# Optimization experiments

Measured on AMD Instinct MI355X. Metric: run time of the kernel, lower is better.

## Reference

```python
import jax, jax.numpy as jnp
import numpy as np

DIM_IN, DIM_Q, DIM_K = 1024, 128, 128
B, S = 8, 2048

def setup_inputs() -> dict:
    key = jax.random.key(0)
    ks = jax.random.split(key, 9)
    sq = 1.0 / np.sqrt(DIM_IN)
    return {
        "query": jax.random.normal(ks[0], (B, S, DIM_IN), jnp.float32),
        "key": jax.random.normal(ks[1], (B, S, DIM_IN), jnp.float32),
        "value": jax.random.normal(ks[2], (B, S, DIM_IN), jnp.float32),
        "Wq": jax.random.uniform(ks[3], (DIM_IN, DIM_Q), jnp.float32, -sq, sq),
        "bq": jax.random.uniform(ks[4], (DIM_Q,), jnp.float32, -sq, sq),
        "Wk": jax.random.uniform(ks[5], (DIM_IN, DIM_K), jnp.float32, -sq, sq),
        "bk": jax.random.uniform(ks[6], (DIM_K,), jnp.float32, -sq, sq),
        "Wv": jax.random.uniform(ks[7], (DIM_IN, DIM_K), jnp.float32, -sq, sq),
        "bv": jax.random.uniform(ks[8], (DIM_K,), jnp.float32, -sq, sq),
    }

def reference(query, key, value, Wq, bq, Wk, bk, Wv, bv):
    q = jnp.einsum("bsd,dq->bsq", query, Wq) + bq          # [B,S,Dq]
    k = jnp.einsum("bsd,dk->bsk", key, Wk) + bk            # [B,S,Dk]
    v = jnp.einsum("bsd,dk->bsk", value, Wv) + bv          # [B,S,Dk]
    scale = jnp.asarray(q.shape[-1] ** 0.5, q.dtype)
    scores = jnp.einsum("bqd,bkd->bqk", q, k) / scale      # [B,S,S]
    attn = jax.nn.softmax(scores, axis=-1)
    return jnp.einsum("bqk,bkd->bqd", attn, v)             # [B,S,Dk]
```

## Files before the change

kernel.cpp:

```cpp
#include <hip/hip_runtime.h>

typedef __attribute__((ext_vector_type(8))) short short8;
typedef __attribute__((ext_vector_type(4))) float floatx4;

#define MFMA16(a, b, c) __builtin_amdgcn_mfma_f32_16x16x32_bf16(a, b, c, 0, 0, 0)

__device__ __forceinline__ short f2bf(float f) {
    unsigned int u = __float_as_uint(f);
    u = u + 0x7fffu + ((u >> 16) & 1u);
    return (short)(u >> 16);
}

__device__ __forceinline__ void ldst16(const void* g, void* l) {
    __builtin_amdgcn_global_load_lds(
        (const __attribute__((address_space(1))) void*)g,
        (__attribute__((address_space(3))) void*)l, 16, 0, 0);
}

__global__ __launch_bounds__(256) void wconv_kernel(const float* __restrict__ Wq,
                                                    const float* __restrict__ Wk,
                                                    const float* __restrict__ Wv,
                                                    short* __restrict__ wtf) {
    int idx = blockIdx.x * 256 + threadIdx.x;
    int w = idx >> 17;
    int rem = idx & 131071;
    int ks = rem >> 12;
    int r2 = rem & 4095;
    int nt = r2 >> 9;
    int r3 = r2 & 511;
    int lane = r3 >> 3, e = r3 & 7;
    int q4 = lane >> 4, l16 = lane & 15;
    int n = 16 * nt + l16;
    int k = 32 * ks + 8 * q4 + e;
    const float* W = (w == 0) ? Wq : (w == 1) ? Wk : Wv;
    wtf[idx] = f2bf(W[k * 128 + n]);
}

__global__ __launch_bounds__(256, 3) void proj_kernel(const float* __restrict__ Q,
                                                      const float* __restrict__ K,
                                                      const float* __restrict__ V,
                                                      const short* __restrict__ wtf,
                                                      const float* __restrict__ bq,
                                                      const float* __restrict__ bk,
                                                      const float* __restrict__ bv,
                                                      short* __restrict__ qo,
                                                      short* __restrict__ ko,
                                                      short* __restrict__ vo) {
    alignas(16) __shared__ float Asl[2][64 * 64];
    const int t = threadIdx.x;
    const int wv = t >> 6, L = t & 63;
    const int wm = wv >> 1, wn = wv & 1;
    const int q4 = L >> 4, l16 = L & 15;
    const int which = blockIdx.y;
    const float* A = (which == 0) ? Q : (which == 1) ? K : V;
    const short* Wf = wtf + which * 131072;
    const float* bias = (which == 0) ? bq : (which == 1) ? bk : bv;
    const int m0 = blockIdx.x * 64;

    floatx4 acc[2][4];
#pragma unroll
    for (int rg = 0; rg < 2; rg++)
#pragma unroll
        for (int nt = 0; nt < 4; nt++) acc[rg][nt] = (floatx4)0.0f;

    auto stage = [&](int buf, int k0) {
#pragma unroll
        for (int j = 0; j < 4; j++) {
            int s = j * 256 + t;
            int r = s >> 4, c = (s & 15) ^ (r & 15);
            ldst16(A + (size_t)(m0 + r) * 1024 + k0 + (c << 2),
                   &Asl[buf][(j * 256 + 64 * wv) * 4]);
        }
    };

    stage(0, 0);

    for (int kc = 0; kc < 16; kc++) {
        const int cur = kc & 1;
        __syncthreads();

        short8 bfr[2][4];
#pragma unroll
        for (int ks = 0; ks < 2; ks++)
#pragma unroll
            for (int nt = 0; nt < 4; nt++)
                bfr[ks][nt] = *(const short8*)(Wf +
                    (((size_t)(2 * kc + ks) * 8 + 4 * wn + nt) * 64 + L) * 8);

        if (kc + 1 < 16) stage(cur ^ 1, (kc + 1) * 64);

        short8 af[2][2];
#pragma unroll
        for (int rg = 0; rg < 2; rg++)
#pragma unroll
            for (int ks = 0; ks < 2; ks++) {
                int r = 32 * wm + 16 * rg + l16;
                int c0 = 8 * ks + 2 * q4;
                float4 f0 = *(float4*)&Asl[cur][(r * 16 + (c0 ^ l16)) * 4];
                float4 f1 = *(float4*)&Asl[cur][(r * 16 + ((c0 + 1) ^ l16)) * 4];
                short8 v;
                v[0] = f2bf(f0.x); v[1] = f2bf(f0.y); v[2] = f2bf(f0.z); v[3] = f2bf(f0.w);
                v[4] = f2bf(f1.x); v[5] = f2bf(f1.y); v[6] = f2bf(f1.z); v[7] = f2bf(f1.w);
                af[rg][ks] = v;
            }
#pragma unroll
        for (int ks = 0; ks < 2; ks++)
#pragma unroll
            for (int nt = 0; nt < 4; nt++) {
                acc[0][nt] = MFMA16(af[0][ks], bfr[ks][nt], acc[0][nt]);
                acc[1][nt] = MFMA16(af[1][ks], bfr[ks][nt], acc[1][nt]);
            }
    }

#pragma unroll
    for (int rg = 0; rg < 2; rg++) {
        const int rbase = m0 + 32 * wm + 16 * rg + q4 * 4;
#pragma unroll
        for (int nt = 0; nt < 4; nt++) {
            const int col = 64 * wn + 16 * nt + l16;
            float bvv = bias[col];
#pragma unroll
            for (int r = 0; r < 4; r++) {
                short h = f2bf(acc[rg][nt][r] + bvv);
                int grow = rbase + r;
                if (which == 0) {
                    qo[(size_t)grow * 128 + col] = h;
                } else if (which == 1) {
                    ko[(size_t)grow * 128 + col] = h;
                } else {
                    int bb = grow >> 11, s = grow & 2047;
                    vo[(size_t)bb * 262144 + (size_t)col * 2048 + s] = h;
                }
            }
        }
    }
}

__global__ __launch_bounds__(512, 2) void flash_kernel(const short* __restrict__ qw,
                                                       const short* __restrict__ kw,
                                                       const short* __restrict__ vw,
                                                       float* __restrict__ out) {
    alignas(16) __shared__ short Kls[2][2][64 * 128];
    alignas(16) __shared__ short Vls[2][2][128 * 64];
    alignas(16) __shared__ short Pl[2][64][72];
    const int t = threadIdx.x;
    const int wvi = t >> 6, L = t & 63;
    const int pr = wvi >> 2, wq = wvi & 3;
    const int pt = t & 255;
    const int q4 = L >> 4, l16 = L & 15;
    const int bid = blockIdx.x;
    const int b = bid & 7, bq = bid >> 3;
    const short* qp = qw + (size_t)b * 262144 + (size_t)bq * 64 * 128;
    const short* kp = kw + (size_t)b * 262144;
    const short* vp = vw + (size_t)b * 262144;

    short8 qf[4];
#pragma unroll
    for (int ks = 0; ks < 4; ks++)
        qf[ks] = *(const short8*)(qp + (16 * wq + l16) * 128 + ks * 32 + q4 * 8);

    floatx4 oacc[8];
#pragma unroll
    for (int dt = 0; dt < 8; dt++) oacc[dt] = (floatx4)0.0f;
    float ps[4] = {0.f, 0.f, 0.f, 0.f};
    const float SL = (float)(0.08838834764831845 * 1.4426950408889634);

    auto stage = [&](int buf, int kt) {
        const int kv0 = pr * 1024 + kt * 64;
#pragma unroll
        for (int j = 0; j < 4; j++) {
            int s = j * 256 + pt;
            int r = s >> 4, c = (s & 15) ^ (r & 15);
            ldst16(kp + (size_t)(kv0 + r) * 128 + c * 8,
                   &Kls[buf][pr][(j * 256 + 64 * wq) * 8]);
        }
#pragma unroll
        for (int j = 0; j < 4; j++) {
            int s = j * 256 + pt;
            int r = s >> 3, c = (s & 7) ^ (r & 7);
            ldst16(vp + (size_t)r * 2048 + kv0 + c * 8,
                   &Vls[buf][pr][(j * 256 + 64 * wq) * 8]);
        }
    };

    stage(0, 0);

    for (int kt = 0; kt < 16; kt++) {
        const int cur = kt & 1;
        __syncthreads();
        if (kt + 1 < 16) stage(cur ^ 1, kt + 1);

        floatx4 sa[4];
#pragma unroll
        for (int nt = 0; nt < 4; nt++) {
            sa[nt] = (floatx4)0.0f;
#pragma unroll
            for (int ks = 0; ks < 4; ks++) {
                short8 bfr = *(short8*)&Kls[cur][pr][(16 * nt + l16) * 128 + ((4 * ks + q4) ^ l16) * 8];
                sa[nt] = MFMA16(qf[ks], bfr, sa[nt]);
            }
        }

#pragma unroll
        for (int nt = 0; nt < 4; nt++) {
#pragma unroll
            for (int r = 0; r < 4; r++) {
                float pv = __builtin_amdgcn_exp2f(sa[nt][r] * SL - 4.0f);
                ps[r] += pv;
                Pl[pr][16 * wq + q4 * 4 + r][16 * nt + l16] = f2bf(pv);
            }
        }

        short8 pf0 = *(short8*)&Pl[pr][16 * wq + l16][q4 * 8];
        short8 pf1 = *(short8*)&Pl[pr][16 * wq + l16][32 + q4 * 8];
#pragma unroll
        for (int dt = 0; dt < 8; dt++) {
            short8 v0 = *(short8*)&Vls[cur][pr][(16 * dt + l16) * 64 + (q4 ^ (l16 & 7)) * 8];
            short8 v1 = *(short8*)&Vls[cur][pr][(16 * dt + l16) * 64 + ((4 + q4) ^ (l16 & 7)) * 8];
            oacc[dt] = MFMA16(pf0, v0, oacc[dt]);
            oacc[dt] = MFMA16(pf1, v1, oacc[dt]);
        }
    }

#pragma unroll
    for (int r = 0; r < 4; r++)
#pragma unroll
        for (int off = 1; off <= 8; off <<= 1)
            ps[r] += __shfl_xor(ps[r], off, 64);

    __syncthreads();
    float* Om = (float*)&Kls[0][0][0];
    float* Lm = (float*)&Vls[0][0][0];
    if (pr == 1) {
#pragma unroll
        for (int dt = 0; dt < 8; dt++)
#pragma unroll
            for (int r = 0; r < 4; r++)
                Om[(16 * wq + q4 * 4 + r) * 128 + 16 * dt + l16] = oacc[dt][r];
        if (l16 == 0)
#pragma unroll
            for (int r = 0; r < 4; r++)
                Lm[16 * wq + q4 * 4 + r] = ps[r];
    }
    __syncthreads();
    if (pr == 0) {
        float inv[4];
#pragma unroll
        for (int r = 0; r < 4; r++)
            inv[r] = 1.0f / (ps[r] + Lm[16 * wq + q4 * 4 + r]);
#pragma unroll
        for (int dt = 0; dt < 8; dt++) {
#pragma unroll
            for (int r = 0; r < 4; r++) {
                int row = 16 * wq + q4 * 4 + r;
                int qrow = bq * 64 + row;
                out[((size_t)b * 2048 + qrow) * 128 + 16 * dt + l16] =
                    (oacc[dt][r] + Om[row * 128 + 16 * dt + l16]) * inv[r];
            }
        }
    }
}

extern "C" void kernel_launch(void* const* d_in, const int* in_sizes, int n_in,
                              void* d_out, int out_size, void* d_ws, size_t ws_size,
                              hipStream_t stream) {
    const float* query = (const float*)d_in[0];
    const float* key   = (const float*)d_in[1];
    const float* value = (const float*)d_in[2];
    const float* Wq    = (const float*)d_in[3];
    const float* bq    = (const float*)d_in[4];
    const float* Wk    = (const float*)d_in[5];
    const float* bk    = (const float*)d_in[6];
    const float* Wv    = (const float*)d_in[7];
    const float* bv    = (const float*)d_in[8];
    float* out = (float*)d_out;

    short* wtf = (short*)d_ws;
    short* qws = wtf + 3 * 131072;
    short* kws = qws + 16384 * 128;
    short* vws = kws + 16384 * 128;

    wconv_kernel<<<1536, 256, 0, stream>>>(Wq, Wk, Wv, wtf);
    proj_kernel<<<dim3(256, 3), 256, 0, stream>>>(query, key, value, wtf,
                                                  bq, bk, bv, qws, kws, vws);
    flash_kernel<<<256, 512, 0, stream>>>(qws, kws, vws, out);
}
```

Baseline: 261.3 us.

## Software-pipeline projection and attention loops with explicit vmcnt waits and setprio

Restructures both the projection GEMM and the attention loop so that the next tile's async LDS loads (and, in the projection, the next weight fragments in a double-buffered register set) are issued before a partial s_waitcnt vmcnt. Raw barriers and sched_barriers replace __syncthreads, and MFMA sections are wrapped in s_setprio to favour matrix issue across waves. The aim is to overlap global-memory latency with compute instead of stalling on a full wait each iteration. This adds hand-counted vmcnt values that must match the number of outstanding loads exactly. It also adds a second barrier per iteration and more register pressure from the two weight buffers.

```diff
diff --git a/kernel.cpp b/kernel.cpp
--- a/kernel.cpp
+++ b/kernel.cpp
@@ -73,22 +73,16 @@
         }
     };
 
-    stage(0, 0);
-
-    for (int kc = 0; kc < 16; kc++) {
-        const int cur = kc & 1;
-        __syncthreads();
-
-        short8 bfr[2][4];
+    auto loadB = [&](int kc, short8 (&dst)[2][4]) {
 #pragma unroll
         for (int ks = 0; ks < 2; ks++)
 #pragma unroll
             for (int nt = 0; nt < 4; nt++)
-                bfr[ks][nt] = *(const short8*)(Wf +
+                dst[ks][nt] = *(const short8*)(Wf +
                     (((size_t)(2 * kc + ks) * 8 + 4 * wn + nt) * 64 + L) * 8);
-
-        if (kc + 1 < 16) stage(cur ^ 1, (kc + 1) * 64);
-
+    };
+
+    auto computeC = [&](int kc, short8 (&bfr)[2][4]) {
         short8 af[2][2];
 #pragma unroll
         for (int rg = 0; rg < 2; rg++)
@@ -96,13 +90,14 @@
             for (int ks = 0; ks < 2; ks++) {
                 int r = 32 * wm + 16 * rg + l16;
                 int c0 = 8 * ks + 2 * q4;
-                float4 f0 = *(float4*)&Asl[cur][(r * 16 + (c0 ^ l16)) * 4];
-                float4 f1 = *(float4*)&Asl[cur][(r * 16 + ((c0 + 1) ^ l16)) * 4];
+                float4 f0 = *(float4*)&Asl[kc & 1][(r * 16 + (c0 ^ l16)) * 4];
+                float4 f1 = *(float4*)&Asl[kc & 1][(r * 16 + ((c0 + 1) ^ l16)) * 4];
                 short8 v;
                 v[0] = f2bf(f0.x); v[1] = f2bf(f0.y); v[2] = f2bf(f0.z); v[3] = f2bf(f0.w);
                 v[4] = f2bf(f1.x); v[5] = f2bf(f1.y); v[6] = f2bf(f1.z); v[7] = f2bf(f1.w);
                 af[rg][ks] = v;
             }
+        __builtin_amdgcn_s_setprio(1);
 #pragma unroll
         for (int ks = 0; ks < 2; ks++)
 #pragma unroll
@@ -110,7 +105,35 @@
                 acc[0][nt] = MFMA16(af[0][ks], bfr[ks][nt], acc[0][nt]);
                 acc[1][nt] = MFMA16(af[1][ks], bfr[ks][nt], acc[1][nt]);
             }
-    }
+        __builtin_amdgcn_s_setprio(0);
+    };
+
+    short8 bA[2][4], bB[2][4];
+
+#define PROJ_STEP(KC, BUSE, BLOAD)                                          \
+    {                                                                       \
+        if ((KC) + 1 < 16) {                                                \
+            stage(((KC) + 1) & 1, ((KC) + 1) * 64);                         \
+            loadB((KC) + 1, BLOAD);                                         \
+            asm volatile("s_waitcnt vmcnt(12)" ::: "memory");               \
+        } else {                                                            \
+            asm volatile("s_waitcnt vmcnt(0)" ::: "memory");                \
+        }                                                                   \
+        __builtin_amdgcn_s_barrier();                                       \
+        __builtin_amdgcn_sched_barrier(0);                                  \
+        computeC((KC), BUSE);                                               \
+        __builtin_amdgcn_sched_barrier(0);                                  \
+        __builtin_amdgcn_s_barrier();                                       \
+    }
+
+    stage(0, 0);
+    loadB(0, bA);
+
+    for (int kc = 0; kc < 16; kc += 2) {
+        PROJ_STEP(kc, bA, bB);
+        PROJ_STEP(kc + 1, bB, bA);
+    }
+#undef PROJ_STEP
 
 #pragma unroll
     for (int rg = 0; rg < 2; rg++) {
@@ -185,12 +208,19 @@
 
     stage(0, 0);
 
+    int cur = 0;
     for (int kt = 0; kt < 16; kt++) {
-        const int cur = kt & 1;
-        __syncthreads();
-        if (kt + 1 < 16) stage(cur ^ 1, kt + 1);
+        if (kt + 1 < 16) {
+            stage(cur ^ 1, kt + 1);
+            asm volatile("s_waitcnt vmcnt(8)" ::: "memory");
+        } else {
+            asm volatile("s_waitcnt vmcnt(0)" ::: "memory");
+        }
+        __builtin_amdgcn_s_barrier();
+        __builtin_amdgcn_sched_barrier(0);
 
         floatx4 sa[4];
+        __builtin_amdgcn_s_setprio(1);
 #pragma unroll
         for (int nt = 0; nt < 4; nt++) {
             sa[nt] = (floatx4)0.0f;
@@ -200,6 +230,7 @@
                 sa[nt] = MFMA16(qf[ks], bfr, sa[nt]);
             }
         }
+        __builtin_amdgcn_s_setprio(0);
 
 #pragma unroll
         for (int nt = 0; nt < 4; nt++) {
@@ -213,6 +244,7 @@
 
         short8 pf0 = *(short8*)&Pl[pr][16 * wq + l16][q4 * 8];
         short8 pf1 = *(short8*)&Pl[pr][16 * wq + l16][32 + q4 * 8];
+        __builtin_amdgcn_s_setprio(1);
 #pragma unroll
         for (int dt = 0; dt < 8; dt++) {
             short8 v0 = *(short8*)&Vls[cur][pr][(16 * dt + l16) * 64 + (q4 ^ (l16 & 7)) * 8];
@@ -220,6 +252,11 @@
             oacc[dt] = MFMA16(pf0, v0, oacc[dt]);
             oacc[dt] = MFMA16(pf1, v1, oacc[dt]);
         }
+        __builtin_amdgcn_s_setprio(0);
+
+        __builtin_amdgcn_sched_barrier(0);
+        __builtin_amdgcn_s_barrier();
+        cur ^= 1;
     }
 
 #pragma unroll
```

Result: no change. 265.1 us (+1.4%).
